# Kernel tuning notes

Hardware: AMD Instinct MI355X
Metric: run time of the kernel (lower is better)

Reference implementation:

```python
import jax, jax.numpy as jnp
import numpy as np

B, T, E, NH = 32, 512, 128, 16
HD = E // NH


def setup_inputs() -> dict:
    key = jax.random.key(0)
    ks = jax.random.split(key, 20)
    s = 0.05
    inp = {
        'anchor_input': jax.random.normal(ks[0], (B, T, 4), jnp.float32),
        'pos_input': jax.random.normal(ks[1], (B, T, 4), jnp.float32),
        'neg_input': jax.random.normal(ks[2], (B, T, 4), jnp.float32),
        'anchor_len': jax.random.randint(ks[3], (B,), 1, T + 1, jnp.int32),
        'pos_len': jax.random.randint(ks[4], (B,), 1, T + 1, jnp.int32),
        'neg_len': jax.random.randint(ks[5], (B,), 1, T + 1, jnp.int32),
        # GRUCell(input_size=2, hidden=128)
        'gru_w_ih': jax.random.normal(ks[6], (3 * E, 2), jnp.float32) * s,
        'gru_w_hh': jax.random.normal(ks[7], (3 * E, E), jnp.float32) * s,
        'gru_b_ih': jax.random.normal(ks[8], (3 * E,), jnp.float32) * s,
        'gru_b_hh': jax.random.normal(ks[9], (3 * E,), jnp.float32) * s,
        # lookup = Linear(2, 128); position_result = Linear(2, 128)
        'lookup_w': jax.random.normal(ks[10], (E, 2), jnp.float32) * s,
        'lookup_b': jax.random.normal(ks[11], (E,), jnp.float32) * s,
        'posres_w': jax.random.normal(ks[12], (E, 2), jnp.float32) * s,
        'posres_b': jax.random.normal(ks[13], (E,), jnp.float32) * s,
        # MultiheadAttention(128, 16)
        'attn_in_w': jax.random.normal(ks[14], (3 * E, E), jnp.float32) * s,
        'attn_in_b': jax.random.normal(ks[15], (3 * E,), jnp.float32) * s,
        'attn_out_w': jax.random.normal(ks[16], (E, E), jnp.float32) * s,
        'attn_out_b': jax.random.normal(ks[17], (E,), jnp.float32) * s,
        'gamma': jnp.float32(0.5),
    }
    return inp


def _sin_pos_emb(x):
    # FixedAbsolutePositionEmbedding with hidden_size=2, type='fixed':
    # x + [sin(pos), cos(pos)] (inv_freq for dim 2 is just 1.0)
    pos = jnp.arange(x.shape[1], dtype=x.dtype)
    pe = jnp.stack([jnp.sin(pos), jnp.cos(pos)], axis=-1)  # [T, 2]
    return x + pe[None, :, :]


def _gru_last(x, lens, w_ih, w_hh, b_ih, b_hh):
    # x: [B, T, 2] -> last valid hidden per torch GRUCell math
    xg = jnp.einsum('btf,gf->btg', x, w_ih) + b_ih  # [B, T, 3E]

    def step(h, xg_t):
        hg = h @ w_hh.T + b_hh
        xr, xz, xn = jnp.split(xg_t, 3, axis=-1)
        hr, hz, hn = jnp.split(hg, 3, axis=-1)
        r = jax.nn.sigmoid(xr + hr)
        z = jax.nn.sigmoid(xz + hz)
        n = jnp.tanh(xn + r * hn)
        h2 = (1.0 - z) * n + z * h
        return h2, h2

    h0 = jnp.zeros((x.shape[0], w_hh.shape[1]), x.dtype)
    _, outs = jax.lax.scan(step, h0, jnp.swapaxes(xg, 0, 1))  # [T, B, E]
    return outs[lens - 1, jnp.arange(x.shape[0])]  # [B, E]


def _mha(x, in_w, in_b, out_w, out_b):
    qkv = x @ in_w.T + in_b  # [B, T, 3E]
    q, k, v = jnp.split(qkv, 3, axis=-1)
    q = q.reshape(B, T, NH, HD)
    k = k.reshape(B, T, NH, HD)
    v = v.reshape(B, T, NH, HD)
    scores = jnp.einsum('bqhd,bkhd->bhqk', q, k) / np.sqrt(HD).astype(np.float32)
    attn = jax.nn.softmax(scores, axis=-1)
    o = jnp.einsum('bhqk,bkhd->bqhd', attn, v).reshape(B, T, E)
    return o @ out_w.T + out_b


def _embed(inp, lens, p):
    coor, grid = inp[:, :, :2], inp[:, :, 2:]
    coor_embs = _gru_last(coor, lens, p['gru_w_ih'], p['gru_w_hh'], p['gru_b_ih'], p['gru_b_hh'])
    sig = grid @ p['lookup_w'].T + p['lookup_b']
    posg = _sin_pos_emb(grid) @ p['posres_w'].T + p['posres_b']
    m = sig + posg  # [B, T, E]
    attn = _mha(m, p['attn_in_w'], p['attn_in_b'], p['attn_out_w'], p['attn_out_b'])
    grid_embs = jnp.mean(attn, axis=1)
    g = p['gamma']
    return g * coor_embs + (1.0 - g) * grid_embs


def reference(anchor_input, pos_input, neg_input, anchor_len, pos_len, neg_len,
              gru_w_ih, gru_w_hh, gru_b_ih, gru_b_hh, lookup_w, lookup_b,
              posres_w, posres_b, attn_in_w, attn_in_b, attn_out_w, attn_out_b, gamma):
    p = dict(gru_w_ih=gru_w_ih, gru_w_hh=gru_w_hh, gru_b_ih=gru_b_ih, gru_b_hh=gru_b_hh,
             lookup_w=lookup_w, lookup_b=lookup_b, posres_w=posres_w, posres_b=posres_b,
             attn_in_w=attn_in_w, attn_in_b=attn_in_b, attn_out_w=attn_out_w,
             attn_out_b=attn_out_b, gamma=gamma)
    a = _embed(anchor_input, anchor_len, p)
    pe = _embed(pos_input, pos_len, p)
    ne = _embed(neg_input, neg_len, p)
    eps = 1e-6  # matches F.pairwise_distance eps
    pos_d = jnp.exp(-jnp.sqrt(jnp.sum((a - pe + eps) ** 2, axis=-1)))
    neg_d = jnp.exp(-jnp.sqrt(jnp.sum((a - ne + eps) ** 2, axis=-1)))
    return ((a, pe, ne), (pos_d, neg_d))
```

## Files before the change

kernel.cpp:

```cpp
#include <hip/hip_runtime.h>
#include <math.h>

#define BB 32
#define TT 512
#define EE 128
#define NHH 16
#define HDD 8
#define G3 384
#define NGRU 96
#define NATT 1536

typedef __attribute__((ext_vector_type(2))) _Float16 half2_t;
typedef __attribute__((ext_vector_type(8))) _Float16 half8_t;

__device__ __forceinline__ float sigmoidf_(float x) {
  return __builtin_amdgcn_rcpf(1.0f + __expf(-x));
}

__device__ __forceinline__ float exp2_(float x) {
#if __has_builtin(__builtin_amdgcn_exp2f)
  return __builtin_amdgcn_exp2f(x);
#else
  return exp2f(x);
#endif
}

__device__ __forceinline__ float fdot2_(half2_t a, half2_t b, float c) {
#if __has_builtin(__builtin_amdgcn_fdot2)
  return __builtin_amdgcn_fdot2(a, b, c, false);
#else
  return fmaf((float)a[0], (float)b[0], fmaf((float)a[1], (float)b[1], c));
#endif
}

#define SC5(p, m, n) \
  fmaf((p).x, (m).x, fmaf((p).y, (m).y, fmaf((p).z, (m).z, fmaf((p).w, (m).w, (n)))))

__global__ __launch_bounds__(512) void coef_kernel(
    const float* __restrict__ attn_in_w, const float* __restrict__ attn_in_b,
    const float* __restrict__ lookup_w, const float* __restrict__ lookup_b,
    const float* __restrict__ posres_w, const float* __restrict__ posres_b,
    float* __restrict__ coef, float* __restrict__ Mh) {
  int j = threadIdx.x;
  __shared__ float cL[5][G3];
  if (j < G3) {
    float u0 = 0.f, u1 = 0.f, cs = 0.f, cc = 0.f, cb = 0.f;
    const float* wrow = attn_in_w + j * EE;
    for (int e = 0; e < EE; ++e) {
      float w = wrow[e];
      float pw0 = posres_w[e * 2], pw1 = posres_w[e * 2 + 1];
      u0 += w * (lookup_w[e * 2] + pw0);
      u1 += w * (lookup_w[e * 2 + 1] + pw1);
      cs += w * pw0;
      cc += w * pw1;
      cb += w * (lookup_b[e] + posres_b[e]);
    }
    cb += attn_in_b[j];
    coef[0 * G3 + j] = u0;
    coef[1 * G3 + j] = u1;
    coef[2 * G3 + j] = cs;
    coef[3 * G3 + j] = cc;
    coef[4 * G3 + j] = cb;
    cL[0][j] = u0;
    cL[1][j] = u1;
    cL[2][j] = cs;
    cL[3][j] = cc;
    cL[4][j] = cb;
  }
  __syncthreads();
  if (j < NHH * 25) {
    int h = j / 25;
    int ij = j % 25;
    int i = ij / 5, jj = ij % 5;
    const float SCL = 0.35355339059327373f * 1.4426950408889634f;
    float acc = 0.f;
#pragma unroll
    for (int d = 0; d < HDD; ++d)
      acc += cL[i][h * HDD + d] * cL[jj][EE + h * HDD + d];
    Mh[h * 25 + ij] = acc * SCL;
  }
}

__global__ __launch_bounds__(512) void fused_kernel(
    const float* __restrict__ in0, const float* __restrict__ in1,
    const float* __restrict__ in2, const int* __restrict__ len0,
    const int* __restrict__ len1, const int* __restrict__ len2,
    const float* __restrict__ w_ih, const float* __restrict__ w_hh,
    const float* __restrict__ b_ih, const float* __restrict__ b_hh,
    const float* __restrict__ coef, const float* __restrict__ Mh,
    float* __restrict__ coor_embs, float* __restrict__ ohat) {
  int tid = threadIdx.x;
  if (blockIdx.x < NGRU) {
    int blk = blockIdx.x;
    int s = blk >> 5;
    int b = blk & 31;
    const float* inp = (s == 0) ? in0 : (s == 1) ? in1 : in2;
    const int* lenp = (s == 0) ? len0 : (s == 1) ? len1 : len2;
    int len = lenp[b];
    int e = tid >> 2;
    int kp = tid & 3;

    __shared__ __align__(16) _Float16 hbh[2][EE];
    __shared__ __align__(16) float xst[TT * 2];

    {
      float4 v = *(const float4*)(inp + ((size_t)b * TT + tid) * 4);
      xst[tid * 2] = v.x;
      xst[tid * 2 + 1] = v.y;
    }
    if (tid < EE) hbh[0][tid] = (_Float16)0.0f;

    int rr = e, rz = e + 128, rn = e + 256;
    half2_t wr[16], wz[16], wn[16];
    {
      const float4* pr = (const float4*)(w_hh + (size_t)rr * EE + 32 * kp);
      const float4* pz = (const float4*)(w_hh + (size_t)rz * EE + 32 * kp);
      const float4* pn = (const float4*)(w_hh + (size_t)rn * EE + 32 * kp);
#pragma unroll
      for (int i = 0; i < 8; ++i) {
        float4 a = pr[i];
        wr[2 * i][0] = (_Float16)a.x; wr[2 * i][1] = (_Float16)a.y;
        wr[2 * i + 1][0] = (_Float16)a.z; wr[2 * i + 1][1] = (_Float16)a.w;
        float4 c = pz[i];
        wz[2 * i][0] = (_Float16)c.x; wz[2 * i][1] = (_Float16)c.y;
        wz[2 * i + 1][0] = (_Float16)c.z; wz[2 * i + 1][1] = (_Float16)c.w;
        float4 d = pn[i];
        wn[2 * i][0] = (_Float16)d.x; wn[2 * i][1] = (_Float16)d.y;
        wn[2 * i + 1][0] = (_Float16)d.z; wn[2 * i + 1][1] = (_Float16)d.w;
      }
    }
    float br = b_ih[rr] + b_hh[rr];
    float bz = b_ih[rz] + b_hh[rz];
    float bn = b_ih[rn];
    float bhn = b_hh[rn];
    float wir0 = w_ih[rr * 2], wir1 = w_ih[rr * 2 + 1];
    float wiz0 = w_ih[rz * 2], wiz1 = w_ih[rz * 2 + 1];
    float win0 = w_ih[rn * 2], win1 = w_ih[rn * 2 + 1];

    float hold = 0.0f;
    __syncthreads();

#pragma unroll 1
    for (int t = 0; t < len; ++t) {
      const half8_t* hp = (const half8_t*)(hbh[t & 1] + 32 * kp);
      half8_t H0 = hp[0], H1 = hp[1], H2 = hp[2], H3 = hp[3];
      half2_t h2[16];
#pragma unroll
      for (int m = 0; m < 4; ++m) {
        h2[m][0] = H0[2 * m]; h2[m][1] = H0[2 * m + 1];
        h2[4 + m][0] = H1[2 * m]; h2[4 + m][1] = H1[2 * m + 1];
        h2[8 + m][0] = H2[2 * m]; h2[8 + m][1] = H2[2 * m + 1];
        h2[12 + m][0] = H3[2 * m]; h2[12 + m][1] = H3[2 * m + 1];
      }
      float x0 = xst[t * 2], x1 = xst[t * 2 + 1];

      float ar0 = 0.f, ar1 = 0.f, az0 = 0.f, az1 = 0.f, an0 = 0.f, an1 = 0.f;
#pragma unroll
      for (int jj = 0; jj < 16; jj += 2) {
        ar0 = fdot2_(wr[jj], h2[jj], ar0);
        ar1 = fdot2_(wr[jj + 1], h2[jj + 1], ar1);
        az0 = fdot2_(wz[jj], h2[jj], az0);
        az1 = fdot2_(wz[jj + 1], h2[jj + 1], az1);
        an0 = fdot2_(wn[jj], h2[jj], an0);
        an1 = fdot2_(wn[jj + 1], h2[jj + 1], an1);
      }
      float hr = ar0 + ar1, hz = az0 + az1, hn = an0 + an1;

      hr += __shfl_xor(hr, 1);
      hz += __shfl_xor(hz, 1);
      hn += __shfl_xor(hn, 1);
      hr += __shfl_xor(hr, 2);
      hz += __shfl_xor(hz, 2);
      hn += __shfl_xor(hn, 2);

      float r = sigmoidf_(br + wir0 * x0 + wir1 * x1 + hr);
      float z = sigmoidf_(bz + wiz0 * x0 + wiz1 * x1 + hz);
      float targ = bn + win0 * x0 + win1 * x1 + r * (bhn + hn);
      float ex = __expf(2.0f * targ);
      float n = 1.0f - 2.0f * __builtin_amdgcn_rcpf(ex + 1.0f);
      hold = n + z * (hold - n);
      if (kp == 0) hbh[(t & 1) ^ 1][e] = (_Float16)hold;
      __syncthreads();
    }
    if (kp == 0) coor_embs[(size_t)blk * EE + e] = hold;
  } else {
    int abk = blockIdx.x - NGRU;
    int s = abk >> 9;
    int bh = abk & 511;
    int b = bh >> 4;
    int h = bh & 15;
    const float* inp = (s == 0) ? in0 : (s == 1) ? in1 : in2;

    __shared__ __align__(16) float4 phiL[TT];
    __shared__ __align__(16) float4 mk4L[TT];
    __shared__ float mk1L[TT];
    __shared__ float red[8][4];

    float M[25];
#pragma unroll
    for (int i = 0; i < 25; ++i) M[i] = Mh[h * 25 + i];

    {
      int t = tid;
      float ft = (float)t;
      float st = sinf(ft);
      float ct = cosf(ft);
      float4 g = *(const float4*)(inp + ((size_t)b * TT + t) * 4);
      float4 phi = make_float4(g.z, g.w, st, ct);
      phiL[t] = phi;
      float m0 = fmaf(M[0], phi.x, fmaf(M[1], phi.y, fmaf(M[2], phi.z, fmaf(M[3], phi.w, M[4]))));
      float m1 = fmaf(M[5], phi.x, fmaf(M[6], phi.y, fmaf(M[7], phi.z, fmaf(M[8], phi.w, M[9]))));
      float m2 = fmaf(M[10], phi.x, fmaf(M[11], phi.y, fmaf(M[12], phi.z, fmaf(M[13], phi.w, M[14]))));
      float m3 = fmaf(M[15], phi.x, fmaf(M[16], phi.y, fmaf(M[17], phi.z, fmaf(M[18], phi.w, M[19]))));
      float m4 = fmaf(M[20], phi.x, fmaf(M[21], phi.y, fmaf(M[22], phi.z, fmaf(M[23], phi.w, M[24]))));
      mk4L[t] = make_float4(m0, m1, m2, m3);
      mk1L[t] = m4;
    }
    __syncthreads();

    float od0, od1, od2, od3;
    {
      float4 p0 = phiL[tid];
      float Z0 = 0.f;
      float n00 = 0.f, n01 = 0.f, n02 = 0.f, n03 = 0.f;
#pragma unroll 2
      for (int k = 0; k < TT; ++k) {
        float4 m = mk4L[k];
        float n = mk1L[k];
        float4 f = phiL[k];
        float e0 = exp2_(SC5(p0, m, n));
        Z0 += e0;
        n00 = fmaf(e0, f.x, n00);
        n01 = fmaf(e0, f.y, n01);
        n02 = fmaf(e0, f.z, n02);
        n03 = fmaf(e0, f.w, n03);
      }
      float rz0 = 1.0f / (Z0 * (float)TT);
      od0 = n00 * rz0;
      od1 = n01 * rz0;
      od2 = n02 * rz0;
      od3 = n03 * rz0;
    }
#pragma unroll
    for (int off = 32; off >= 1; off >>= 1) {
      od0 += __shfl_xor(od0, off, 64);
      od1 += __shfl_xor(od1, off, 64);
      od2 += __shfl_xor(od2, off, 64);
      od3 += __shfl_xor(od3, off, 64);
    }
    {
      int wave = tid >> 6;
      int lane = tid & 63;
      if (lane == 0) {
        red[wave][0] = od0;
        red[wave][1] = od1;
        red[wave][2] = od2;
        red[wave][3] = od3;
      }
    }
    __syncthreads();
    if (tid < HDD) {
      float wp0 = 0.f, wp1 = 0.f, wp2 = 0.f, wp3 = 0.f;
#pragma unroll
      for (int w = 0; w < 8; ++w) {
        wp0 += red[w][0];
        wp1 += red[w][1];
        wp2 += red[w][2];
        wp3 += red[w][3];
      }
      int jv = 2 * EE + h * HDD + tid;
      float o = coef[jv] * wp0 + coef[G3 + jv] * wp1 + coef[2 * G3 + jv] * wp2 +
                coef[3 * G3 + jv] * wp3 + coef[4 * G3 + jv];
      ohat[(size_t)abk * HDD + tid] = o;
    }
  }
}

__global__ __launch_bounds__(128) void finalize_kernel(
    const float* __restrict__ attn_out_w, const float* __restrict__ attn_out_b,
    const float* __restrict__ ohat, const float* __restrict__ coor_embs,
    const float* __restrict__ gamma_p, float* __restrict__ out) {
  int blk = blockIdx.x;
  int e = threadIdx.x;
  __shared__ float ov[EE];
  ov[e] = ohat[(size_t)blk * EE + e];
  __syncthreads();
  float acc = attn_out_b[e];
  const float* wrow = attn_out_w + (size_t)e * EE;
#pragma unroll 8
  for (int f = 0; f < EE; ++f) acc += wrow[f] * ov[f];
  float g = gamma_p[0];
  out[(size_t)blk * EE + e] = g * coor_embs[(size_t)blk * EE + e] + (1.0f - g) * acc;
}

__global__ void dist_kernel(float* __restrict__ out) {
  int i = threadIdx.x;
  int b = i & 31;
  int neg = i >> 5;
  const float* a = out + (size_t)b * EE;
  const float* x = out + (size_t)(1 + neg) * BB * EE + (size_t)b * EE;
  float sum = 0.f;
  for (int e = 0; e < EE; ++e) {
    float d = a[e] - x[e] + 1e-6f;
    sum += d * d;
  }
  out[3 * BB * EE + neg * BB + b] = expf(-sqrtf(sum));
}

extern "C" void kernel_launch(void* const* d_in, const int* in_sizes, int n_in,
                              void* d_out, int out_size, void* d_ws, size_t ws_size,
                              hipStream_t stream) {
  const float* a_in = (const float*)d_in[0];
  const float* p_in = (const float*)d_in[1];
  const float* ng_in = (const float*)d_in[2];
  const int* a_len = (const int*)d_in[3];
  const int* p_len = (const int*)d_in[4];
  const int* ng_len = (const int*)d_in[5];
  const float* w_ih = (const float*)d_in[6];
  const float* w_hh = (const float*)d_in[7];
  const float* b_ih = (const float*)d_in[8];
  const float* b_hh = (const float*)d_in[9];
  const float* lookup_w = (const float*)d_in[10];
  const float* lookup_b = (const float*)d_in[11];
  const float* posres_w = (const float*)d_in[12];
  const float* posres_b = (const float*)d_in[13];
  const float* attn_in_w = (const float*)d_in[14];
  const float* attn_in_b = (const float*)d_in[15];
  const float* attn_out_w = (const float*)d_in[16];
  const float* attn_out_b = (const float*)d_in[17];
  const float* gamma_p = (const float*)d_in[18];
  float* out = (float*)d_out;

  float* coef = (float*)d_ws;
  float* Mh = coef + 2048;
  float* ohat = Mh + 512;
  float* cemb = ohat + 12288;

  hipLaunchKernelGGL(coef_kernel, dim3(1), dim3(512), 0, stream, attn_in_w,
                     attn_in_b, lookup_w, lookup_b, posres_w, posres_b, coef, Mh);
  hipLaunchKernelGGL(fused_kernel, dim3(NGRU + NATT), dim3(512), 0, stream, a_in,
                     p_in, ng_in, a_len, p_len, ng_len, w_ih, w_hh, b_ih, b_hh,
                     coef, Mh, cemb, ohat);
  hipLaunchKernelGGL(finalize_kernel, dim3(96), dim3(128), 0, stream, attn_out_w,
                     attn_out_b, ohat, cemb, gamma_p, out);
  hipLaunchKernelGGL(dist_kernel, dim3(1), dim3(64), 0, stream, out);
}
```

Before: 292.6 us.

## Map one wave per attention head and register-block eight queries per lane

Attention blocks now cover eight heads each, one head per wave, instead of one head per 512-thread block, so the attention grid drops from 1536 to 192 blocks. Each lane holds eight query rows in registers and computes the key projection on the fly inside the loop, instead of precomputing it into shared memory. This removes the shared key arrays, the cross-wave reduction and one barrier, and lets one phi load serve eight queries. In exchange it raises register pressure and leaves far fewer blocks to share the GPU with the GRU blocks.

```diff
diff --git a/kernel.cpp b/kernel.cpp
--- a/kernel.cpp
+++ b/kernel.cpp
@@ -8,7 +8,7 @@
 #define HDD 8
 #define G3 384
 #define NGRU 96
-#define NATT 1536
+#define NATT 192
 
 typedef __attribute__((ext_vector_type(2))) _Float16 half2_t;
 typedef __attribute__((ext_vector_type(8))) _Float16 half8_t;
@@ -32,9 +32,6 @@
   return fmaf((float)a[0], (float)b[0], fmaf((float)a[1], (float)b[1], c));
 #endif
 }
-
-#define SC5(p, m, n) \
-  fmaf((p).x, (m).x, fmaf((p).y, (m).y, fmaf((p).z, (m).z, fmaf((p).w, (m).w, (n)))))
 
 __global__ __launch_bounds__(512) void coef_kernel(
     const float* __restrict__ attn_in_w, const float* __restrict__ attn_in_b,
@@ -184,21 +181,17 @@
     }
     if (kp == 0) coor_embs[(size_t)blk * EE + e] = hold;
   } else {
-    int abk = blockIdx.x - NGRU;
-    int s = abk >> 9;
-    int bh = abk & 511;
-    int b = bh >> 4;
-    int h = bh & 15;
+    int a = blockIdx.x - NGRU;
+    int s = a / 64;
+    int rem = a - s * 64;
+    int b = rem >> 1;
+    int hg = rem & 1;
     const float* inp = (s == 0) ? in0 : (s == 1) ? in1 : in2;
+    int wave = tid >> 6;
+    int lane = tid & 63;
+    int h = hg * 8 + wave;
 
     __shared__ __align__(16) float4 phiL[TT];
-    __shared__ __align__(16) float4 mk4L[TT];
-    __shared__ float mk1L[TT];
-    __shared__ float red[8][4];
-
-    float M[25];
-#pragma unroll
-    for (int i = 0; i < 25; ++i) M[i] = Mh[h * 25 + i];
 
     {
       int t = tid;
@@ -206,40 +199,52 @@
       float st = sinf(ft);
       float ct = cosf(ft);
       float4 g = *(const float4*)(inp + ((size_t)b * TT + t) * 4);
-      float4 phi = make_float4(g.z, g.w, st, ct);
-      phiL[t] = phi;
-      float m0 = fmaf(M[0], phi.x, fmaf(M[1], phi.y, fmaf(M[2], phi.z, fmaf(M[3], phi.w, M[4]))));
-      float m1 = fmaf(M[5], phi.x, fmaf(M[6], phi.y, fmaf(M[7], phi.z, fmaf(M[8], phi.w, M[9]))));
-      float m2 = fmaf(M[10], phi.x, fmaf(M[11], phi.y, fmaf(M[12], phi.z, fmaf(M[13], phi.w, M[14]))));
-      float m3 = fmaf(M[15], phi.x, fmaf(M[16], phi.y, fmaf(M[17], phi.z, fmaf(M[18], phi.w, M[19]))));
-      float m4 = fmaf(M[20], phi.x, fmaf(M[21], phi.y, fmaf(M[22], phi.z, fmaf(M[23], phi.w, M[24]))));
-      mk4L[t] = make_float4(m0, m1, m2, m3);
-      mk1L[t] = m4;
-    }
+      phiL[t] = make_float4(g.z, g.w, st, ct);
+    }
+
+    float M[25];
+#pragma unroll
+    for (int i = 0; i < 25; ++i) M[i] = Mh[h * 25 + i];
     __syncthreads();
 
-    float od0, od1, od2, od3;
-    {
-      float4 p0 = phiL[tid];
-      float Z0 = 0.f;
-      float n00 = 0.f, n01 = 0.f, n02 = 0.f, n03 = 0.f;
-#pragma unroll 2
-      for (int k = 0; k < TT; ++k) {
-        float4 m = mk4L[k];
-        float n = mk1L[k];
-        float4 f = phiL[k];
-        float e0 = exp2_(SC5(p0, m, n));
-        Z0 += e0;
-        n00 = fmaf(e0, f.x, n00);
-        n01 = fmaf(e0, f.y, n01);
-        n02 = fmaf(e0, f.z, n02);
-        n03 = fmaf(e0, f.w, n03);
+    float4 p[8];
+#pragma unroll
+    for (int j = 0; j < 8; ++j) p[j] = phiL[lane + 64 * j];
+
+    float Z[8];
+    float N0[8], N1[8], N2[8], N3[8];
+#pragma unroll
+    for (int j = 0; j < 8; ++j) {
+      Z[j] = 0.f; N0[j] = 0.f; N1[j] = 0.f; N2[j] = 0.f; N3[j] = 0.f;
+    }
+
+#pragma unroll 1
+    for (int k = 0; k < TT; ++k) {
+      float4 f = phiL[k];
+      float m0 = fmaf(M[0], f.x, fmaf(M[1], f.y, fmaf(M[2], f.z, fmaf(M[3], f.w, M[4]))));
+      float m1 = fmaf(M[5], f.x, fmaf(M[6], f.y, fmaf(M[7], f.z, fmaf(M[8], f.w, M[9]))));
+      float m2 = fmaf(M[10], f.x, fmaf(M[11], f.y, fmaf(M[12], f.z, fmaf(M[13], f.w, M[14]))));
+      float m3 = fmaf(M[15], f.x, fmaf(M[16], f.y, fmaf(M[17], f.z, fmaf(M[18], f.w, M[19]))));
+      float m4 = fmaf(M[20], f.x, fmaf(M[21], f.y, fmaf(M[22], f.z, fmaf(M[23], f.w, M[24]))));
+#pragma unroll
+      for (int j = 0; j < 8; ++j) {
+        float e0 = exp2_(fmaf(p[j].x, m0, fmaf(p[j].y, m1, fmaf(p[j].z, m2, fmaf(p[j].w, m3, m4)))));
+        Z[j] += e0;
+        N0[j] = fmaf(e0, f.x, N0[j]);
+        N1[j] = fmaf(e0, f.y, N1[j]);
+        N2[j] = fmaf(e0, f.z, N2[j]);
+        N3[j] = fmaf(e0, f.w, N3[j]);
       }
-      float rz0 = 1.0f / (Z0 * (float)TT);
-      od0 = n00 * rz0;
-      od1 = n01 * rz0;
-      od2 = n02 * rz0;
-      od3 = n03 * rz0;
+    }
+
+    float od0 = 0.f, od1 = 0.f, od2 = 0.f, od3 = 0.f;
+#pragma unroll
+    for (int j = 0; j < 8; ++j) {
+      float rz = __builtin_amdgcn_rcpf(Z[j] * (float)TT);
+      od0 = fmaf(N0[j], rz, od0);
+      od1 = fmaf(N1[j], rz, od1);
+      od2 = fmaf(N2[j], rz, od2);
+      od3 = fmaf(N3[j], rz, od3);
     }
 #pragma unroll
     for (int off = 32; off >= 1; off >>= 1) {
@@ -248,30 +253,12 @@
       od2 += __shfl_xor(od2, off, 64);
       od3 += __shfl_xor(od3, off, 64);
     }
-    {
-      int wave = tid >> 6;
-      int lane = tid & 63;
-      if (lane == 0) {
-        red[wave][0] = od0;
-        red[wave][1] = od1;
-        red[wave][2] = od2;
-        red[wave][3] = od3;
-      }
-    }
-    __syncthreads();
-    if (tid < HDD) {
-      float wp0 = 0.f, wp1 = 0.f, wp2 = 0.f, wp3 = 0.f;
-#pragma unroll
-      for (int w = 0; w < 8; ++w) {
-        wp0 += red[w][0];
-        wp1 += red[w][1];
-        wp2 += red[w][2];
-        wp3 += red[w][3];
-      }
-      int jv = 2 * EE + h * HDD + tid;
-      float o = coef[jv] * wp0 + coef[G3 + jv] * wp1 + coef[2 * G3 + jv] * wp2 +
-                coef[3 * G3 + jv] * wp3 + coef[4 * G3 + jv];
-      ohat[(size_t)abk * HDD + tid] = o;
+    if (lane < HDD) {
+      int jv = 2 * EE + h * HDD + lane;
+      float o = coef[jv] * od0 + coef[G3 + jv] * od1 + coef[2 * G3 + jv] * od2 +
+                coef[3 * G3 + jv] * od3 + coef[4 * G3 + jv];
+      int abk = s * 512 + b * 16 + h;
+      ohat[(size_t)abk * HDD + lane] = o;
     }
   }
 }
```

New measurement: 355.4 us. 1.21x slower.
